# Kernel optimization log

Hardware: AMD Instinct MI355X
Metric: run time of the kernel (lower is better)

The kernel has to match this reference:

```python
import jax, jax.numpy as jnp
import numpy as np
from jax import lax

B, N, S, NSAMPLE = 8, 4096, 1024, 32
RADIUS = 0.2
EPS = 1e-5
IN_CH = 64
MLP = [64, 64, 128]


def _fps(xyz, npoint):
    # farthest point sampling; deterministic start at index 0 (torch uses a random start)
    b, n, _ = xyz.shape
    bidx = jnp.arange(b)

    def step(carry, _):
        distance, farthest = carry
        centroid = xyz[bidx, farthest][:, None, :]            # [B,1,3]
        d = jnp.sum((xyz - centroid) ** 2, axis=-1)           # [B,N]
        distance = jnp.minimum(distance, d)
        nxt = jnp.argmax(distance, axis=-1).astype(jnp.int32)
        return (distance, nxt), farthest

    init = (jnp.full((b, n), 1e10, dtype=xyz.dtype), jnp.zeros((b,), jnp.int32))
    _, idxs = lax.scan(step, init, None, length=npoint)
    return idxs.T                                             # [B,npoint]


def _index_points(p, idx):
    # p: [B,N,C], idx: [B,...] -> [B,...,C]
    return jax.vmap(lambda pp, ii: pp[ii])(p, idx)


def _square_distance(src, dst):
    # src [B,S,3], dst [B,N,3] -> [B,S,N]
    d = -2.0 * jnp.einsum('bsc,bnc->bsn', src, dst)
    d += jnp.sum(src ** 2, -1)[:, :, None]
    d += jnp.sum(dst ** 2, -1)[:, None, :]
    return d


def _query_ball(radius, nsample, xyz, new_xyz):
    n = xyz.shape[1]
    sqr = _square_distance(new_xyz, xyz)                      # [B,S,N]
    gidx = jnp.where(sqr > radius ** 2, n, jnp.arange(n, dtype=jnp.int32))
    gidx = jnp.sort(gidx, axis=-1)[:, :, :nsample]            # [B,S,nsample]
    first = gidx[:, :, :1]
    return jnp.where(gidx == n, first, gidx)


def setup_inputs() -> dict:
    key = jax.random.key(0)
    ks = jax.random.split(key, 8)
    inp = {
        'xyz': jax.random.uniform(ks[0], (B, N, 3), jnp.float32),
        'points': jax.random.normal(ks[1], (B, N, IN_CH), jnp.float32),
    }
    last = IN_CH + 3
    for i, out_c in enumerate(MLP):
        scale = 1.0 / np.sqrt(last)
        inp[f'w{i}'] = jax.random.normal(ks[2 + i], (out_c, last), jnp.float32) * scale
        inp[f'b{i}'] = jnp.zeros((out_c,), jnp.float32)
        inp[f'g{i}'] = jnp.ones((out_c,), jnp.float32)
        inp[f'be{i}'] = jnp.zeros((out_c,), jnp.float32)
        last = out_c
    return inp


def _forward(xyz, points, params):
    fps_idx = _fps(xyz, S)
    new_xyz = _index_points(xyz, fps_idx)                     # [B,S,3]
    idx = _query_ball(RADIUS, NSAMPLE, xyz, new_xyz)          # [B,S,n]
    grouped_xyz = _index_points(xyz, idx) - new_xyz[:, :, None, :]
    h = jnp.concatenate([grouped_xyz, _index_points(points, idx)], axis=-1)  # [B,S,n,67]
    for (w, b, g, be) in params:
        h = jnp.einsum('bsnc,oc->bsno', h, w) + b             # 1x1 conv
        mu = jnp.mean(h, axis=(0, 1, 2))
        var = jnp.var(h, axis=(0, 1, 2))                      # training-mode batch norm
        h = jax.nn.relu((h - mu) * lax.rsqrt(var + EPS) * g + be)
    new_points = jnp.max(h, axis=2)                           # [B,S,Cout]
    return new_xyz, jnp.transpose(new_points, (0, 2, 1))      # [B,Cout,S] like torch


def reference(xyz, points, w0, b0, g0, be0, w1, b1, g1, be1, w2, b2, g2, be2):
    params = [(w0, b0, g0, be0), (w1, b1, g1, be1), (w2, b2, g2, be2)]
    return _forward(xyz, points, params)
```

## Files before the change

kernel.cpp:

```cpp
#include <hip/hip_runtime.h>
#include <stdint.h>

#define NB 8
#define NPTS 4096
#define NS 1024
#define NK 32
#define NROWS (NB*NS*NK)
#define R2 0.04f
#define NCOPY 32

typedef __attribute__((ext_vector_type(8))) short bf16x8;
typedef __attribute__((ext_vector_type(4))) float f32x4;
typedef __attribute__((ext_vector_type(2))) float f32x2;

__device__ __forceinline__ float bf2f(uint16_t u){
    uint32_t v = ((uint32_t)u) << 16;
    return __uint_as_float(v);
}
__device__ __forceinline__ uint16_t f2bf(float f){
    uint32_t u = __float_as_uint(f);
    uint32_t r = (u + 0x7FFFu + ((u >> 16) & 1u)) >> 16;
    return (uint16_t)r;
}
__device__ __forceinline__ bf16x8 load_bf8(const uint16_t* p){
    return *reinterpret_cast<const bf16x8*>(p);
}

#define DPPMAX64(key, ctrl, rmask)                                             \
    {                                                                          \
        uint32_t _lo = (uint32_t)(key), _hi = (uint32_t)((key) >> 32);         \
        uint32_t _olo = (uint32_t)__builtin_amdgcn_update_dpp(                 \
            0, (int)_lo, (ctrl), (rmask), 0xf, true);                          \
        uint32_t _ohi = (uint32_t)__builtin_amdgcn_update_dpp(                 \
            0, (int)_hi, (ctrl), (rmask), 0xf, true);                          \
        unsigned long long _o = (((unsigned long long)_ohi) << 32) | _olo;     \
        key = (_o > (key)) ? _o : (key);                                       \
    }

#define FT 16
__global__ __launch_bounds__(256) void fps_kernel(const float* __restrict__ xyz,
                                                  float* __restrict__ out_newxyz){
    __shared__ float LX[NPTS], LY[NPTS], LZ[NPTS];
    __shared__ float4 SC[NS];
    __shared__ alignas(16) unsigned long long cand[2][4];
    const int b = blockIdx.x, t = threadIdx.x;
    const float* base = xyz + (size_t)b * (NPTS*3);
    f32x2 px2[FT/2], py2[FT/2], pz2[FT/2], pd2[FT/2];
#pragma unroll
    for (int j = 0; j < FT/2; ++j){
        int i = t*FT + 2*j;
        float x0 = base[i*3+0], y0 = base[i*3+1], z0 = base[i*3+2];
        float x1 = base[i*3+3], y1 = base[i*3+4], z1 = base[i*3+5];
        px2[j] = (f32x2){x0, x1};
        py2[j] = (f32x2){y0, y1};
        pz2[j] = (f32x2){z0, z1};
        pd2[j] = (f32x2){1e10f, 1e10f};
        LX[i]=x0; LY[i]=y0; LZ[i]=z0;
        LX[i+1]=x1; LY[i+1]=y1; LZ[i+1]=z1;
    }
    __syncthreads();
    int cur = 0;
    const int wave = t >> 6, lane = t & 63;
    for (int s = 0; s < NS; ++s){
        float cx = LX[cur], cy = LY[cur], cz = LZ[cur];
        if (t == 0) SC[s] = make_float4(cx, cy, cz, 0.f);
        f32x2 ncx = (f32x2){-cx, -cx};
        f32x2 ncy = (f32x2){-cy, -cy};
        f32x2 ncz = (f32x2){-cz, -cz};
        float bestd = -1.0f; int besti = 0;
#pragma unroll
        for (int j = 0; j < FT/2; ++j){
            f32x2 d2;
            {
#pragma clang fp contract(off)
                f32x2 dx = px2[j] + ncx;
                f32x2 dy = py2[j] + ncy;
                f32x2 dz = pz2[j] + ncz;
                f32x2 xx = dx*dx, yy = dy*dy, zz = dz*dz;
                d2 = (xx + yy) + zz;
            }
            f32x2 nd;
            nd.x = fminf(pd2[j].x, d2.x);
            nd.y = fminf(pd2[j].y, d2.y);
            pd2[j] = nd;
            if (nd.x > bestd){ bestd = nd.x; besti = t*FT + 2*j; }
            if (nd.y > bestd){ bestd = nd.y; besti = t*FT + 2*j + 1; }
        }
        unsigned long long key =
            (((unsigned long long)__float_as_uint(bestd)) << 32) |
            (unsigned long long)(~(unsigned)besti);
        DPPMAX64(key, 0x111, 0xf);
        DPPMAX64(key, 0x112, 0xf);
        DPPMAX64(key, 0x114, 0xf);
        DPPMAX64(key, 0x118, 0xf);
        DPPMAX64(key, 0x142, 0xa);
        DPPMAX64(key, 0x143, 0xc);
        int p = s & 1;
        if (lane == 63) cand[p][wave] = key;
        __syncthreads();
        ulonglong2 c01 = *reinterpret_cast<const ulonglong2*>(&cand[p][0]);
        ulonglong2 c23 = *reinterpret_cast<const ulonglong2*>(&cand[p][2]);
        unsigned long long m01 = (c01.x > c01.y) ? c01.x : c01.y;
        unsigned long long m23 = (c23.x > c23.y) ? c23.x : c23.y;
        unsigned long long km  = (m01 > m23) ? m01 : m23;
        cur = (int)(~(uint32_t)km);
    }
    __syncthreads();
    for (int i = t; i < NS; i += 256){
        float4 c = SC[i];
        float* o = out_newxyz + ((size_t)b*NS + i)*3;
        o[0] = c.x; o[1] = c.y; o[2] = c.z;
    }
}

__global__ __launch_bounds__(256) void qball_kernel(const float* __restrict__ xyz,
                                                    const float* __restrict__ newxyz,
                                                    int* __restrict__ idx_out){
    int gid = blockIdx.x*256 + threadIdx.x;
    int w = gid >> 6, lane = gid & 63;
    int b = w >> 10;
    const float* q = newxyz + (size_t)w*3;
    float qx = q[0], qy = q[1], qz = q[2];
    float qn = qx*qx;
    qn = fmaf(qy, qy, qn);
    qn = fmaf(qz, qz, qn);
    const float* base = xyz + (size_t)b * (NPTS*3);
    int cnt = 0, first = 0;
    for (int c0 = 0; c0 < NPTS; c0 += 64){
        int i = c0 + lane;
        float x = base[i*3+0], y = base[i*3+1], z = base[i*3+2];
        float xn = x*x;
        xn = fmaf(y, y, xn);
        xn = fmaf(z, z, xn);
        float dot = qx*x;
        dot = fmaf(qy, y, dot);
        dot = fmaf(qz, z, dot);
        float d;
        {
#pragma clang fp contract(off)
            d = -2.0f * dot;
            d = d + qn;
            d = d + xn;
        }
        bool in = !(d > R2);
        unsigned long long m = __ballot(in);
        if (in){
            int rank = __popcll(m & ((1ull << lane) - 1ull));
            int pos = cnt + rank;
            if (pos < NK) idx_out[(size_t)w*NK + pos] = i;
        }
        if (cnt == 0 && m) first = c0 + (__ffsll((unsigned long long)m) - 1);
        cnt += __popcll(m);
        if (cnt >= NK) break;
    }
    if (cnt < NK){
        for (int p = cnt + lane; p < NK; p += 64) idx_out[(size_t)w*NK + p] = first;
    }
}

__global__ void prep_kernel(const float* __restrict__ w0, const float* __restrict__ w1,
                            const float* __restrict__ w2, uint16_t* __restrict__ w0b,
                            uint16_t* __restrict__ w1b, uint16_t* __restrict__ w2b,
                            double* __restrict__ accumAll){
    int t = blockIdx.x*256 + threadIdx.x;
    int stride = gridDim.x*256;
    for (int i = t; i < 3*NCOPY*256; i += stride) accumAll[i] = 0.0;
    for (int i = t; i < 64*96; i += stride){
        int n = i/96, c = i%96;
        w0b[i] = (c < 67) ? f2bf(w0[n*67 + c]) : (uint16_t)0;
    }
    for (int i = t; i < 64*64; i += stride)  w1b[i] = f2bf(w1[i]);
    for (int i = t; i < 128*64; i += stride) w2b[i] = f2bf(w2[i]);
}

__global__ __launch_bounds__(256) void layer0_mfma(const float* __restrict__ xyz,
                                                   const float* __restrict__ pts,
                                                   const int* __restrict__ idx,
                                                   const float* __restrict__ newxyz,
                                                   const uint16_t* __restrict__ w0b,
                                                   const float* __restrict__ b0,
                                                   uint16_t* __restrict__ z0,
                                                   double* __restrict__ accumOut){
    __shared__ float S_s[16][64], S_q[16][64];
    const int wave = threadIdx.x >> 6, lane = threadIdx.x & 63;
    const int q = lane >> 4, l16 = lane & 15;
    const int r0 = blockIdx.x*64 + wave*16;
    const int row = r0 + l16;
    const int b = row >> 15;
    const int bs = row >> 5;
    const int id = idx[row];
    const float* prow = pts + (((size_t)b << 12) + id)*64;
    const float* xr   = xyz + (((size_t)b << 12) + id)*3;
    const float* qr   = newxyz + (size_t)bs*3;
    float d0 = xr[0]-qr[0], d1 = xr[1]-qr[1], d2 = xr[2]-qr[2];

    bf16x8 Bf[4][3];
#pragma unroll
    for (int nt = 0; nt < 4; ++nt)
#pragma unroll
        for (int s = 0; s < 3; ++s)
            Bf[nt][s] = load_bf8(w0b + (nt*16 + l16)*96 + s*32 + q*8);

    f32x4 acc[4];
#pragma unroll
    for (int nt = 0; nt < 4; ++nt) acc[nt] = (f32x4){0.f,0.f,0.f,0.f};

#pragma unroll
    for (int s = 0; s < 3; ++s){
        const int k0 = s*32 + q*8;
        bf16x8 a;
#pragma unroll
        for (int j = 0; j < 8; ++j){
            int k = k0 + j;
            float v = (k < 3) ? ((k == 0) ? d0 : ((k == 1) ? d1 : d2))
                              : ((k < 67) ? prow[k-3] : 0.f);
            a[j] = (short)f2bf(v);
        }
#pragma unroll
        for (int nt = 0; nt < 4; ++nt)
            acc[nt] = __builtin_amdgcn_mfma_f32_16x16x32_bf16(a, Bf[nt][s], acc[nt], 0, 0, 0);
    }
#pragma unroll
    for (int nt = 0; nt < 4; ++nt){
        int c = nt*16 + l16;
        float bb = b0[c];
        float sps = 0.f, spq = 0.f;
#pragma unroll
        for (int reg = 0; reg < 4; ++reg){
            int rr = r0 + q*4 + reg;
            float h = acc[nt][reg] + bb;
            sps += h;
            spq = fmaf(h, h, spq);
            z0[(size_t)rr*64 + c] = f2bf(h);
        }
        S_s[wave*4 + q][c] = sps;
        S_q[wave*4 + q][c] = spq;
    }
    __syncthreads();
    int t = threadIdx.x;
    if (t < 64){
        double ss = 0.0, sq = 0.0;
#pragma unroll
        for (int i = 0; i < 16; ++i){ ss += (double)S_s[i][t]; sq += (double)S_q[i][t]; }
        int cp = blockIdx.x & (NCOPY-1);
        atomicAdd(&accumOut[cp*256 + t], ss);
        atomicAdd(&accumOut[cp*256 + 128 + t], sq);
    }
}

__global__ __launch_bounds__(256) void layer1_mfma(const uint16_t* __restrict__ zin,
                                                   const double* __restrict__ accumIn,
                                                   const float* __restrict__ g,
                                                   const float* __restrict__ be,
                                                   const uint16_t* __restrict__ wb,
                                                   const float* __restrict__ bias,
                                                   uint16_t* __restrict__ zout,
                                                   double* __restrict__ accumOut){
    constexpr int NT = 4;
    __shared__ float sc_l[64], sh_l[64];
    __shared__ float S_s[16][64], S_q[16][64];
    const int t = threadIdx.x;
    if (t < 64){
        double s = 0.0, qq = 0.0;
#pragma unroll
        for (int cp = 0; cp < NCOPY; ++cp){
            s  += accumIn[cp*256 + t];
            qq += accumIn[cp*256 + 128 + t];
        }
        double mean = s / (double)NROWS;
        double var  = qq / (double)NROWS - mean*mean;
        double rs = 1.0 / sqrt(var + 1e-5);
        double scv = (double)g[t] * rs;
        sc_l[t] = (float)scv;
        sh_l[t] = (float)((double)be[t] - mean*scv);
    }
    __syncthreads();

    const int wave = t >> 6, lane = t & 63;
    const int q = lane >> 4, l16 = lane & 15;
    const int r0 = blockIdx.x*64 + wave*16;

    bf16x8 Bf[NT][2];
#pragma unroll
    for (int nt = 0; nt < NT; ++nt)
#pragma unroll
        for (int s = 0; s < 2; ++s)
            Bf[nt][s] = load_bf8(wb + (nt*16 + l16)*64 + s*32 + q*8);

    float sc[2][8], sh[2][8];
#pragma unroll
    for (int s = 0; s < 2; ++s)
#pragma unroll
        for (int j = 0; j < 8; ++j){
            sc[s][j] = sc_l[s*32 + q*8 + j];
            sh[s][j] = sh_l[s*32 + q*8 + j];
        }

    f32x4 acc[NT];
#pragma unroll
    for (int nt = 0; nt < NT; ++nt) acc[nt] = (f32x4){0.f,0.f,0.f,0.f};

    const uint16_t* zr = zin + (size_t)(r0 + l16)*64;
#pragma unroll
    for (int s = 0; s < 2; ++s){
        uint4 u = *reinterpret_cast<const uint4*>(zr + s*32 + q*8);
        float h[8];
        h[0] = bf2f((uint16_t)(u.x & 0xFFFF)); h[1] = bf2f((uint16_t)(u.x >> 16));
        h[2] = bf2f((uint16_t)(u.y & 0xFFFF)); h[3] = bf2f((uint16_t)(u.y >> 16));
        h[4] = bf2f((uint16_t)(u.z & 0xFFFF)); h[5] = bf2f((uint16_t)(u.z >> 16));
        h[6] = bf2f((uint16_t)(u.w & 0xFFFF)); h[7] = bf2f((uint16_t)(u.w >> 16));
        bf16x8 a;
#pragma unroll
        for (int j = 0; j < 8; ++j){
            float v = fmaxf(fmaf(h[j], sc[s][j], sh[s][j]), 0.f);
            a[j] = (short)f2bf(v);
        }
#pragma unroll
        for (int nt = 0; nt < NT; ++nt)
            acc[nt] = __builtin_amdgcn_mfma_f32_16x16x32_bf16(a, Bf[nt][s], acc[nt], 0, 0, 0);
    }
#pragma unroll
    for (int nt = 0; nt < NT; ++nt){
        int c = nt*16 + l16;
        float bb = bias[c];
        float sps = 0.f, spq = 0.f;
#pragma unroll
        for (int reg = 0; reg < 4; ++reg){
            int rr = r0 + q*4 + reg;
            float h = acc[nt][reg] + bb;
            sps += h;
            spq = fmaf(h, h, spq);
            zout[(size_t)rr*64 + c] = f2bf(h);
        }
        S_s[wave*4 + q][c] = sps;
        S_q[wave*4 + q][c] = spq;
    }
    __syncthreads();
    if (t < 64){
        double ss = 0.0, sq = 0.0;
#pragma unroll
        for (int i = 0; i < 16; ++i){ ss += (double)S_s[i][t]; sq += (double)S_q[i][t]; }
        int cp = blockIdx.x & (NCOPY-1);
        atomicAdd(&accumOut[cp*256 + t], ss);
        atomicAdd(&accumOut[cp*256 + 128 + t], sq);
    }
}

__global__ __launch_bounds__(256) void layer2_mfma(const uint16_t* __restrict__ zin,
                                                   const double* __restrict__ accumIn,
                                                   const float* __restrict__ g,
                                                   const float* __restrict__ be,
                                                   const uint16_t* __restrict__ wb,
                                                   const float* __restrict__ bias,
                                                   float2* __restrict__ pool,
                                                   double* __restrict__ accumOut){
    constexpr int NT = 8;
    __shared__ float sc_l[64], sh_l[64];
    __shared__ float S_s[16][128], S_q[16][128];
    __shared__ float P_mx[16][128], P_mn[16][128];
    const int t = threadIdx.x;
    if (t < 64){
        double s = 0.0, qq = 0.0;
#pragma unroll
        for (int cp = 0; cp < NCOPY; ++cp){
            s  += accumIn[cp*256 + t];
            qq += accumIn[cp*256 + 128 + t];
        }
        double mean = s / (double)NROWS;
        double var  = qq / (double)NROWS - mean*mean;
        double rs = 1.0 / sqrt(var + 1e-5);
        double scv = (double)g[t] * rs;
        sc_l[t] = (float)scv;
        sh_l[t] = (float)((double)be[t] - mean*scv);
    }
    __syncthreads();

    const int wave = t >> 6, lane = t & 63;
    const int q = lane >> 4, l16 = lane & 15;
    const int r0 = blockIdx.x*64 + wave*16;

    bf16x8 Bf[NT][2];
#pragma unroll
    for (int nt = 0; nt < NT; ++nt)
#pragma unroll
        for (int s = 0; s < 2; ++s)
            Bf[nt][s] = load_bf8(wb + (nt*16 + l16)*64 + s*32 + q*8);

    float sc[2][8], sh[2][8];
#pragma unroll
    for (int s = 0; s < 2; ++s)
#pragma unroll
        for (int j = 0; j < 8; ++j){
            sc[s][j] = sc_l[s*32 + q*8 + j];
            sh[s][j] = sh_l[s*32 + q*8 + j];
        }

    f32x4 acc[NT];
#pragma unroll
    for (int nt = 0; nt < NT; ++nt) acc[nt] = (f32x4){0.f,0.f,0.f,0.f};

    const uint16_t* zr = zin + (size_t)(r0 + l16)*64;
#pragma unroll
    for (int s = 0; s < 2; ++s){
        uint4 u = *reinterpret_cast<const uint4*>(zr + s*32 + q*8);
        float h[8];
        h[0] = bf2f((uint16_t)(u.x & 0xFFFF)); h[1] = bf2f((uint16_t)(u.x >> 16));
        h[2] = bf2f((uint16_t)(u.y & 0xFFFF)); h[3] = bf2f((uint16_t)(u.y >> 16));
        h[4] = bf2f((uint16_t)(u.z & 0xFFFF)); h[5] = bf2f((uint16_t)(u.z >> 16));
        h[6] = bf2f((uint16_t)(u.w & 0xFFFF)); h[7] = bf2f((uint16_t)(u.w >> 16));
        bf16x8 a;
#pragma unroll
        for (int j = 0; j < 8; ++j){
            float v = fmaxf(fmaf(h[j], sc[s][j], sh[s][j]), 0.f);
            a[j] = (short)f2bf(v);
        }
#pragma unroll
        for (int nt = 0; nt < NT; ++nt)
            acc[nt] = __builtin_amdgcn_mfma_f32_16x16x32_bf16(a, Bf[nt][s], acc[nt], 0, 0, 0);
    }
#pragma unroll
    for (int nt = 0; nt < NT; ++nt){
        int c = nt*16 + l16;
        float bb = bias[c];
        float sps = 0.f, spq = 0.f;
        float mx = -1e30f, mn = 1e30f;
#pragma unroll
        for (int reg = 0; reg < 4; ++reg){
            float h = acc[nt][reg] + bb;
            sps += h;
            spq = fmaf(h, h, spq);
            mx = fmaxf(mx, h);
            mn = fminf(mn, h);
        }
        S_s[wave*4 + q][c] = sps;
        S_q[wave*4 + q][c] = spq;
        P_mx[wave*4 + q][c] = mx;
        P_mn[wave*4 + q][c] = mn;
    }
    __syncthreads();
    if (t < 128){
        double ss = 0.0, sq = 0.0;
#pragma unroll
        for (int i = 0; i < 16; ++i){ ss += (double)S_s[i][t]; sq += (double)S_q[i][t]; }
        int cp = blockIdx.x & (NCOPY-1);
        atomicAdd(&accumOut[cp*256 + t], ss);
        atomicAdd(&accumOut[cp*256 + 128 + t], sq);
    }
    {
        int gidx = t >> 7;
        int c = t & 127;
        float mx = -1e30f, mn = 1e30f;
#pragma unroll
        for (int i = 0; i < 8; ++i){
            mx = fmaxf(mx, P_mx[gidx*8 + i][c]);
            mn = fminf(mn, P_mn[gidx*8 + i][c]);
        }
        pool[(size_t)(blockIdx.x*2 + gidx)*128 + c] = make_float2(mx, mn);
    }
}

__global__ __launch_bounds__(256) void final_kernel(const float2* __restrict__ pool,
                                                    const double* __restrict__ accumIn,
                                                    const float* __restrict__ g,
                                                    const float* __restrict__ be,
                                                    float* __restrict__ out){
    __shared__ float sc_l[128], sh_l[128];
    const int t0 = threadIdx.x;
    if (t0 < 128){
        double s = 0.0, qq = 0.0;
#pragma unroll
        for (int cp = 0; cp < NCOPY; ++cp){
            s  += accumIn[cp*256 + t0];
            qq += accumIn[cp*256 + 128 + t0];
        }
        double mean = s / (double)NROWS;
        double var  = qq / (double)NROWS - mean*mean;
        double rs = 1.0 / sqrt(var + 1e-5);
        double scv = (double)g[t0] * rs;
        sc_l[t0] = (float)scv;
        sh_l[t0] = (float)((double)be[t0] - mean*scv);
    }
    __syncthreads();

    int t = blockIdx.x*256 + threadIdx.x;
    int o = t & 127;
    int s = (t >> 7) & 1023;
    int b = t >> 17;
    float2 p = pool[t];
    float sc = sc_l[o], sh = sh_l[o];
    float zsel = (sc >= 0.f) ? p.x : p.y;
    float y = fmaxf(fmaf(zsel, sc, sh), 0.f);
    out[24576 + ((size_t)b << 17) + ((size_t)o << 10) + s] = y;
}

extern "C" void kernel_launch(void* const* d_in, const int* in_sizes, int n_in,
                              void* d_out, int out_size, void* d_ws, size_t ws_size,
                              hipStream_t stream) {
    const float* xyz = (const float*)d_in[0];
    const float* pts = (const float*)d_in[1];
    const float* w0  = (const float*)d_in[2];
    const float* b0  = (const float*)d_in[3];
    const float* g0  = (const float*)d_in[4];
    const float* be0 = (const float*)d_in[5];
    const float* w1  = (const float*)d_in[6];
    const float* b1  = (const float*)d_in[7];
    const float* g1  = (const float*)d_in[8];
    const float* be1 = (const float*)d_in[9];
    const float* w2  = (const float*)d_in[10];
    const float* b2  = (const float*)d_in[11];
    const float* g2  = (const float*)d_in[12];
    const float* be2 = (const float*)d_in[13];
    float* out = (float*)d_out;

    char* ws = (char*)d_ws;
    double*   accum0 = (double*)(ws + 0);
    double*   accum1 = (double*)(ws + 65536);
    double*   accum2 = (double*)(ws + 131072);
    uint16_t* w0b    = (uint16_t*)(ws + 196608);
    uint16_t* w1b    = (uint16_t*)(ws + 208896);
    uint16_t* w2b    = (uint16_t*)(ws + 217088);
    uint16_t* z0     = (uint16_t*)(ws + 262144);
    uint16_t* z1     = (uint16_t*)(ws + 33816576);
    float2*   pool   = (float2*)  (ws + 67371008);
    int*      idx    = (int*)     (ws + 75759616);

    prep_kernel<<<32, 256, 0, stream>>>(w0, w1, w2, w0b, w1b, w2b, accum0);
    fps_kernel<<<NB, 256, 0, stream>>>(xyz, out);
    qball_kernel<<<2048, 256, 0, stream>>>(xyz, out, idx);
    layer0_mfma<<<4096, 256, 0, stream>>>(xyz, pts, idx, out, w0b, b0, z0, accum0);
    layer1_mfma<<<4096, 256, 0, stream>>>(z0, accum0, g0, be0, w1b, b1, z1, accum1);
    layer2_mfma<<<4096, 256, 0, stream>>>(z1, accum1, g1, be1, w2b, b2, pool, accum2);
    final_kernel<<<4096, 256, 0, stream>>>(pool, accum2, g2, be2, out);
}
```

Baseline: 830.4 us.

## Fuse FPS, ball query and layer0 into one persistent producer-consumer kernel

Merges the FPS, ball-query and first MLP layer kernels into one launch. The first 8 blocks run FPS and publish each centroid to global memory with a flag, and the worker blocks spin on those flags. Each worker then runs the ball query for two centroids into shared memory and does the layer0 MFMA right away. The aim is to overlap the long serial FPS with grouping and layer0 work and to drop the idx buffer round trip. It risks deadlock if the FPS blocks are not resident before the spinning workers, and it relies on oversized shared memory to force one block per CU.

```diff
diff --git a/kernel.cpp b/kernel.cpp
--- a/kernel.cpp
+++ b/kernel.cpp
@@ -24,6 +24,25 @@
 }
 __device__ __forceinline__ bf16x8 load_bf8(const uint16_t* p){
     return *reinterpret_cast<const bf16x8*>(p);
+}
+
+__device__ __forceinline__ void publish_cent(float* cent, int cell,
+                                             float cx, float cy, float cz){
+    f32x4 v; v[0] = cx; v[1] = cy; v[2] = cz; v[3] = 1.0f;
+    unsigned long long a = (unsigned long long)(uintptr_t)(cent + (size_t)cell*4);
+    asm volatile("global_store_dwordx4 %0, %1, off sc0 sc1"
+                 :: "v"(a), "v"(v) : "memory");
+}
+__device__ __forceinline__ f32x4 wait_cent(const float* cent, int cell){
+    const uint32_t* wp = (const uint32_t*)(cent + (size_t)cell*4) + 3;
+    while (__hip_atomic_load(wp, __ATOMIC_RELAXED, __HIP_MEMORY_SCOPE_AGENT)
+           != 0x3F800000u)
+        __builtin_amdgcn_s_sleep(32);
+    f32x4 r;
+    unsigned long long a = (unsigned long long)(uintptr_t)(cent + (size_t)cell*4);
+    asm volatile("global_load_dwordx4 %0, %1, off sc0 sc1\n\ts_waitcnt vmcnt(0)"
+                 : "=v"(r) : "v"(a) : "memory");
+    return r;
 }
 
 #define DPPMAX64(key, ctrl, rmask)                                             \
@@ -37,215 +56,235 @@
         key = (_o > (key)) ? _o : (key);                                       \
     }
 
+struct FpsSh {
+    float LX[NPTS], LY[NPTS], LZ[NPTS];
+    f32x4 SC[NS];
+    alignas(16) unsigned long long cand[2][4];
+};
+struct WrkSh {
+    float S_s[16][64], S_q[16][64];
+    int   idxL[2][NK];
+    f32x4 Lc[2];
+};
+union MegaSh { FpsSh f; WrkSh w; char force_one_block_per_cu[86016]; };
+
 #define FT 16
-__global__ __launch_bounds__(256) void fps_kernel(const float* __restrict__ xyz,
-                                                  float* __restrict__ out_newxyz){
-    __shared__ float LX[NPTS], LY[NPTS], LZ[NPTS];
-    __shared__ float4 SC[NS];
-    __shared__ alignas(16) unsigned long long cand[2][4];
-    const int b = blockIdx.x, t = threadIdx.x;
-    const float* base = xyz + (size_t)b * (NPTS*3);
-    f32x2 px2[FT/2], py2[FT/2], pz2[FT/2], pd2[FT/2];
-#pragma unroll
-    for (int j = 0; j < FT/2; ++j){
-        int i = t*FT + 2*j;
-        float x0 = base[i*3+0], y0 = base[i*3+1], z0 = base[i*3+2];
-        float x1 = base[i*3+3], y1 = base[i*3+4], z1 = base[i*3+5];
-        px2[j] = (f32x2){x0, x1};
-        py2[j] = (f32x2){y0, y1};
-        pz2[j] = (f32x2){z0, z1};
-        pd2[j] = (f32x2){1e10f, 1e10f};
-        LX[i]=x0; LY[i]=y0; LZ[i]=z0;
-        LX[i+1]=x1; LY[i+1]=y1; LZ[i+1]=z1;
-    }
-    __syncthreads();
-    int cur = 0;
-    const int wave = t >> 6, lane = t & 63;
-    for (int s = 0; s < NS; ++s){
-        float cx = LX[cur], cy = LY[cur], cz = LZ[cur];
-        if (t == 0) SC[s] = make_float4(cx, cy, cz, 0.f);
-        f32x2 ncx = (f32x2){-cx, -cx};
-        f32x2 ncy = (f32x2){-cy, -cy};
-        f32x2 ncz = (f32x2){-cz, -cz};
-        float bestd = -1.0f; int besti = 0;
+__global__ __launch_bounds__(256) void mega_kernel(const float* __restrict__ xyz,
+                                                   const float* __restrict__ pts,
+                                                   const uint16_t* __restrict__ w0b,
+                                                   const float* __restrict__ b0,
+                                                   uint16_t* __restrict__ z0,
+                                                   double* __restrict__ accumOut,
+                                                   float* __restrict__ cent,
+                                                   float* __restrict__ out_newxyz){
+    __shared__ MegaSh sh;
+    const int t = threadIdx.x;
+
+    if (blockIdx.x < NB){
+        const int b = blockIdx.x;
+        const float* base = xyz + (size_t)b * (NPTS*3);
+        f32x2 px2[FT/2], py2[FT/2], pz2[FT/2], pd2[FT/2];
 #pragma unroll
         for (int j = 0; j < FT/2; ++j){
-            f32x2 d2;
-            {
+            int i = t*FT + 2*j;
+            float x0 = base[i*3+0], y0 = base[i*3+1], z0c = base[i*3+2];
+            float x1 = base[i*3+3], y1 = base[i*3+4], z1c = base[i*3+5];
+            px2[j] = (f32x2){x0, x1};
+            py2[j] = (f32x2){y0, y1};
+            pz2[j] = (f32x2){z0c, z1c};
+            pd2[j] = (f32x2){1e10f, 1e10f};
+            sh.f.LX[i]=x0; sh.f.LY[i]=y0; sh.f.LZ[i]=z0c;
+            sh.f.LX[i+1]=x1; sh.f.LY[i+1]=y1; sh.f.LZ[i+1]=z1c;
+        }
+        __syncthreads();
+        int cur = 0;
+        const int wave = t >> 6, lane = t & 63;
+        for (int s = 0; s < NS; ++s){
+            float cx = sh.f.LX[cur], cy = sh.f.LY[cur], cz = sh.f.LZ[cur];
+            if (t == 0){
+                sh.f.SC[s] = (f32x4){cx, cy, cz, 0.f};
+                publish_cent(cent, b*NS + s, cx, cy, cz);
+            }
+            f32x2 ncx = (f32x2){-cx, -cx};
+            f32x2 ncy = (f32x2){-cy, -cy};
+            f32x2 ncz = (f32x2){-cz, -cz};
+            float bestd = -1.0f; int besti = 0;
+#pragma unroll
+            for (int j = 0; j < FT/2; ++j){
+                f32x2 d2;
+                {
 #pragma clang fp contract(off)
-                f32x2 dx = px2[j] + ncx;
-                f32x2 dy = py2[j] + ncy;
-                f32x2 dz = pz2[j] + ncz;
-                f32x2 xx = dx*dx, yy = dy*dy, zz = dz*dz;
-                d2 = (xx + yy) + zz;
+                    f32x2 dx = px2[j] + ncx;
+                    f32x2 dy = py2[j] + ncy;
+                    f32x2 dz = pz2[j] + ncz;
+                    f32x2 xx = dx*dx, yy = dy*dy, zz = dz*dz;
+                    d2 = (xx + yy) + zz;
+                }
+                f32x2 nd;
+                nd.x = fminf(pd2[j].x, d2.x);
+                nd.y = fminf(pd2[j].y, d2.y);
+                pd2[j] = nd;
+                if (nd.x > bestd){ bestd = nd.x; besti = t*FT + 2*j; }
+                if (nd.y > bestd){ bestd = nd.y; besti = t*FT + 2*j + 1; }
             }
-            f32x2 nd;
-            nd.x = fminf(pd2[j].x, d2.x);
-            nd.y = fminf(pd2[j].y, d2.y);
-            pd2[j] = nd;
-            if (nd.x > bestd){ bestd = nd.x; besti = t*FT + 2*j; }
-            if (nd.y > bestd){ bestd = nd.y; besti = t*FT + 2*j + 1; }
-        }
-        unsigned long long key =
-            (((unsigned long long)__float_as_uint(bestd)) << 32) |
-            (unsigned long long)(~(unsigned)besti);
-        DPPMAX64(key, 0x111, 0xf);
-        DPPMAX64(key, 0x112, 0xf);
-        DPPMAX64(key, 0x114, 0xf);
-        DPPMAX64(key, 0x118, 0xf);
-        DPPMAX64(key, 0x142, 0xa);
-        DPPMAX64(key, 0x143, 0xc);
-        int p = s & 1;
-        if (lane == 63) cand[p][wave] = key;
+            unsigned long long key =
+                (((unsigned long long)__float_as_uint(bestd)) << 32) |
+                (unsigned long long)(~(unsigned)besti);
+            DPPMAX64(key, 0x111, 0xf);
+            DPPMAX64(key, 0x112, 0xf);
+            DPPMAX64(key, 0x114, 0xf);
+            DPPMAX64(key, 0x118, 0xf);
+            DPPMAX64(key, 0x142, 0xa);
+            DPPMAX64(key, 0x143, 0xc);
+            int p = s & 1;
+            if (lane == 63) sh.f.cand[p][wave] = key;
+            __syncthreads();
+            ulonglong2 c01 = *reinterpret_cast<const ulonglong2*>(&sh.f.cand[p][0]);
+            ulonglong2 c23 = *reinterpret_cast<const ulonglong2*>(&sh.f.cand[p][2]);
+            unsigned long long m01 = (c01.x > c01.y) ? c01.x : c01.y;
+            unsigned long long m23 = (c23.x > c23.y) ? c23.x : c23.y;
+            unsigned long long km  = (m01 > m23) ? m01 : m23;
+            cur = (int)(~(uint32_t)km);
+        }
         __syncthreads();
-        ulonglong2 c01 = *reinterpret_cast<const ulonglong2*>(&cand[p][0]);
-        ulonglong2 c23 = *reinterpret_cast<const ulonglong2*>(&cand[p][2]);
-        unsigned long long m01 = (c01.x > c01.y) ? c01.x : c01.y;
-        unsigned long long m23 = (c23.x > c23.y) ? c23.x : c23.y;
-        unsigned long long km  = (m01 > m23) ? m01 : m23;
-        cur = (int)(~(uint32_t)km);
-    }
-    __syncthreads();
-    for (int i = t; i < NS; i += 256){
-        float4 c = SC[i];
-        float* o = out_newxyz + ((size_t)b*NS + i)*3;
-        o[0] = c.x; o[1] = c.y; o[2] = c.z;
-    }
-}
-
-__global__ __launch_bounds__(256) void qball_kernel(const float* __restrict__ xyz,
-                                                    const float* __restrict__ newxyz,
-                                                    int* __restrict__ idx_out){
-    int gid = blockIdx.x*256 + threadIdx.x;
-    int w = gid >> 6, lane = gid & 63;
-    int b = w >> 10;
-    const float* q = newxyz + (size_t)w*3;
-    float qx = q[0], qy = q[1], qz = q[2];
-    float qn = qx*qx;
-    qn = fmaf(qy, qy, qn);
-    qn = fmaf(qz, qz, qn);
-    const float* base = xyz + (size_t)b * (NPTS*3);
-    int cnt = 0, first = 0;
-    for (int c0 = 0; c0 < NPTS; c0 += 64){
-        int i = c0 + lane;
-        float x = base[i*3+0], y = base[i*3+1], z = base[i*3+2];
-        float xn = x*x;
-        xn = fmaf(y, y, xn);
-        xn = fmaf(z, z, xn);
-        float dot = qx*x;
-        dot = fmaf(qy, y, dot);
-        dot = fmaf(qz, z, dot);
-        float d;
-        {
+        for (int i = t; i < NS; i += 256){
+            f32x4 c = sh.f.SC[i];
+            float* o = out_newxyz + ((size_t)b*NS + i)*3;
+            o[0] = c[0]; o[1] = c[1]; o[2] = c[2];
+        }
+    } else {
+        const int w = (int)blockIdx.x - NB;
+        const int stile = w >> 3;
+        const int b = w & 7;
+        const int wave = t >> 6, lane = t & 63;
+        const int q = lane >> 4, l16 = lane & 15;
+
+        bf16x8 Bf[4][3];
+#pragma unroll
+        for (int nt = 0; nt < 4; ++nt)
+#pragma unroll
+            for (int s = 0; s < 3; ++s)
+                Bf[nt][s] = load_bf8(w0b + (nt*16 + l16)*96 + s*32 + q*8);
+
+        if (t == 0){
+            sh.w.Lc[0] = wait_cent(cent, b*NS + stile*2 + 0);
+            sh.w.Lc[1] = wait_cent(cent, b*NS + stile*2 + 1);
+        }
+        __syncthreads();
+
+        if (wave < 2){
+            f32x4 qc = sh.w.Lc[wave];
+            float qx = qc[0], qy = qc[1], qz = qc[2];
+            float qn = qx*qx;
+            qn = fmaf(qy, qy, qn);
+            qn = fmaf(qz, qz, qn);
+            const float* base = xyz + (size_t)b * (NPTS*3);
+            int cnt = 0, first = 0;
+            for (int c0 = 0; c0 < NPTS; c0 += 64){
+                int i = c0 + lane;
+                float x = base[i*3+0], y = base[i*3+1], z = base[i*3+2];
+                float xn = x*x;
+                xn = fmaf(y, y, xn);
+                xn = fmaf(z, z, xn);
+                float dot = qx*x;
+                dot = fmaf(qy, y, dot);
+                dot = fmaf(qz, z, dot);
+                float d;
+                {
 #pragma clang fp contract(off)
-            d = -2.0f * dot;
-            d = d + qn;
-            d = d + xn;
-        }
-        bool in = !(d > R2);
-        unsigned long long m = __ballot(in);
-        if (in){
-            int rank = __popcll(m & ((1ull << lane) - 1ull));
-            int pos = cnt + rank;
-            if (pos < NK) idx_out[(size_t)w*NK + pos] = i;
-        }
-        if (cnt == 0 && m) first = c0 + (__ffsll((unsigned long long)m) - 1);
-        cnt += __popcll(m);
-        if (cnt >= NK) break;
-    }
-    if (cnt < NK){
-        for (int p = cnt + lane; p < NK; p += 64) idx_out[(size_t)w*NK + p] = first;
+                    d = -2.0f * dot;
+                    d = d + qn;
+                    d = d + xn;
+                }
+                bool in = !(d > R2);
+                unsigned long long m = __ballot(in);
+                if (in){
+                    int rank = __popcll(m & ((1ull << lane) - 1ull));
+                    int pos = cnt + rank;
+                    if (pos < NK) sh.w.idxL[wave][pos] = i;
+                }
+                if (cnt == 0 && m) first = c0 + (__ffsll((unsigned long long)m) - 1);
+                cnt += __popcll(m);
+                if (cnt >= NK) break;
+            }
+            if (cnt < NK){
+                for (int p = cnt + lane; p < NK; p += 64) sh.w.idxL[wave][p] = first;
+            }
+        }
+        __syncthreads();
+
+        const int rowbase = (b*NS + stile*2)*NK;
+        const int r0 = rowbase + wave*16;
+        const int cell = wave >> 1;
+        const int sample = (wave & 1)*16 + l16;
+        const int id = sh.w.idxL[cell][sample];
+        const float* prow = pts + (((size_t)b << 12) + id)*64;
+        const float* xr   = xyz + (((size_t)b << 12) + id)*3;
+        f32x4 qc = sh.w.Lc[cell];
+        float d0 = xr[0]-qc[0], d1 = xr[1]-qc[1], d2 = xr[2]-qc[2];
+
+        f32x4 acc[4];
+#pragma unroll
+        for (int nt = 0; nt < 4; ++nt) acc[nt] = (f32x4){0.f,0.f,0.f,0.f};
+
+#pragma unroll
+        for (int s = 0; s < 3; ++s){
+            const int k0 = s*32 + q*8;
+            bf16x8 a;
+#pragma unroll
+            for (int j = 0; j < 8; ++j){
+                int k = k0 + j;
+                float v = (k < 3) ? ((k == 0) ? d0 : ((k == 1) ? d1 : d2))
+                                  : ((k < 67) ? prow[k-3] : 0.f);
+                a[j] = (short)f2bf(v);
+            }
+#pragma unroll
+            for (int nt = 0; nt < 4; ++nt)
+                acc[nt] = __builtin_amdgcn_mfma_f32_16x16x32_bf16(a, Bf[nt][s], acc[nt], 0, 0, 0);
+        }
+#pragma unroll
+        for (int nt = 0; nt < 4; ++nt){
+            int c = nt*16 + l16;
+            float bb = b0[c];
+            float sps = 0.f, spq = 0.f;
+#pragma unroll
+            for (int reg = 0; reg < 4; ++reg){
+                int rr = r0 + q*4 + reg;
+                float h = acc[nt][reg] + bb;
+                sps += h;
+                spq = fmaf(h, h, spq);
+                z0[(size_t)rr*64 + c] = f2bf(h);
+            }
+            sh.w.S_s[wave*4 + q][c] = sps;
+            sh.w.S_q[wave*4 + q][c] = spq;
+        }
+        __syncthreads();
+        if (t < 64){
+            double ss = 0.0, sq = 0.0;
+#pragma unroll
+            for (int i = 0; i < 16; ++i){ ss += (double)sh.w.S_s[i][t]; sq += (double)sh.w.S_q[i][t]; }
+            int cp = blockIdx.x & (NCOPY-1);
+            atomicAdd(&accumOut[cp*256 + t], ss);
+            atomicAdd(&accumOut[cp*256 + 128 + t], sq);
+        }
     }
 }
 
 __global__ void prep_kernel(const float* __restrict__ w0, const float* __restrict__ w1,
                             const float* __restrict__ w2, uint16_t* __restrict__ w0b,
                             uint16_t* __restrict__ w1b, uint16_t* __restrict__ w2b,
-                            double* __restrict__ accumAll){
+                            double* __restrict__ accumAll, float* __restrict__ cent){
     int t = blockIdx.x*256 + threadIdx.x;
     int stride = gridDim.x*256;
     for (int i = t; i < 3*NCOPY*256; i += stride) accumAll[i] = 0.0;
+    for (int i = t; i < NB*NS; i += stride)
+        ((f32x4*)cent)[i] = (f32x4){0.f, 0.f, 0.f, 0.f};
     for (int i = t; i < 64*96; i += stride){
         int n = i/96, c = i%96;
         w0b[i] = (c < 67) ? f2bf(w0[n*67 + c]) : (uint16_t)0;
     }
     for (int i = t; i < 64*64; i += stride)  w1b[i] = f2bf(w1[i]);
     for (int i = t; i < 128*64; i += stride) w2b[i] = f2bf(w2[i]);
-}
-
-__global__ __launch_bounds__(256) void layer0_mfma(const float* __restrict__ xyz,
-                                                   const float* __restrict__ pts,
-                                                   const int* __restrict__ idx,
-                                                   const float* __restrict__ newxyz,
-                                                   const uint16_t* __restrict__ w0b,
-                                                   const float* __restrict__ b0,
-                                                   uint16_t* __restrict__ z0,
-                                                   double* __restrict__ accumOut){
-    __shared__ float S_s[16][64], S_q[16][64];
-    const int wave = threadIdx.x >> 6, lane = threadIdx.x & 63;
-    const int q = lane >> 4, l16 = lane & 15;
-    const int r0 = blockIdx.x*64 + wave*16;
-    const int row = r0 + l16;
-    const int b = row >> 15;
-    const int bs = row >> 5;
-    const int id = idx[row];
-    const float* prow = pts + (((size_t)b << 12) + id)*64;
-    const float* xr   = xyz + (((size_t)b << 12) + id)*3;
-    const float* qr   = newxyz + (size_t)bs*3;
-    float d0 = xr[0]-qr[0], d1 = xr[1]-qr[1], d2 = xr[2]-qr[2];
-
-    bf16x8 Bf[4][3];
-#pragma unroll
-    for (int nt = 0; nt < 4; ++nt)
-#pragma unroll
-        for (int s = 0; s < 3; ++s)
-            Bf[nt][s] = load_bf8(w0b + (nt*16 + l16)*96 + s*32 + q*8);
-
-    f32x4 acc[4];
-#pragma unroll
-    for (int nt = 0; nt < 4; ++nt) acc[nt] = (f32x4){0.f,0.f,0.f,0.f};
-
-#pragma unroll
-    for (int s = 0; s < 3; ++s){
-        const int k0 = s*32 + q*8;
-        bf16x8 a;
-#pragma unroll
-        for (int j = 0; j < 8; ++j){
-            int k = k0 + j;
-            float v = (k < 3) ? ((k == 0) ? d0 : ((k == 1) ? d1 : d2))
-                              : ((k < 67) ? prow[k-3] : 0.f);
-            a[j] = (short)f2bf(v);
-        }
-#pragma unroll
-        for (int nt = 0; nt < 4; ++nt)
-            acc[nt] = __builtin_amdgcn_mfma_f32_16x16x32_bf16(a, Bf[nt][s], acc[nt], 0, 0, 0);
-    }
-#pragma unroll
-    for (int nt = 0; nt < 4; ++nt){
-        int c = nt*16 + l16;
-        float bb = b0[c];
-        float sps = 0.f, spq = 0.f;
-#pragma unroll
-        for (int reg = 0; reg < 4; ++reg){
-            int rr = r0 + q*4 + reg;
-            float h = acc[nt][reg] + bb;
-            sps += h;
-            spq = fmaf(h, h, spq);
-            z0[(size_t)rr*64 + c] = f2bf(h);
-        }
-        S_s[wave*4 + q][c] = sps;
-        S_q[wave*4 + q][c] = spq;
-    }
-    __syncthreads();
-    int t = threadIdx.x;
-    if (t < 64){
-        double ss = 0.0, sq = 0.0;
-#pragma unroll
-        for (int i = 0; i < 16; ++i){ ss += (double)S_s[i][t]; sq += (double)S_q[i][t]; }
-        int cp = blockIdx.x & (NCOPY-1);
-        atomicAdd(&accumOut[cp*256 + t], ss);
-        atomicAdd(&accumOut[cp*256 + 128 + t], sq);
-    }
 }
 
 __global__ __launch_bounds__(256) void layer1_mfma(const uint16_t* __restrict__ zin,
@@ -522,12 +561,10 @@
     uint16_t* z0     = (uint16_t*)(ws + 262144);
     uint16_t* z1     = (uint16_t*)(ws + 33816576);
     float2*   pool   = (float2*)  (ws + 67371008);
-    int*      idx    = (int*)     (ws + 75759616);
-
-    prep_kernel<<<32, 256, 0, stream>>>(w0, w1, w2, w0b, w1b, w2b, accum0);
-    fps_kernel<<<NB, 256, 0, stream>>>(xyz, out);
-    qball_kernel<<<2048, 256, 0, stream>>>(xyz, out, idx);
-    layer0_mfma<<<4096, 256, 0, stream>>>(xyz, pts, idx, out, w0b, b0, z0, accum0);
+    float*    cent   = (float*)   (ws + 75759616);
+
+    prep_kernel<<<32, 256, 0, stream>>>(w0, w1, w2, w0b, w1b, w2b, accum0, cent);
+    mega_kernel<<<NB + 4096, 256, 0, stream>>>(xyz, pts, w0b, b0, z0, accum0, cent, out);
     layer1_mfma<<<4096, 256, 0, stream>>>(z0, accum0, g0, be0, w1b, b1, z1, accum1);
     layer2_mfma<<<4096, 256, 0, stream>>>(z1, accum1, g1, be1, w2b, b2, pool, accum2);
     final_kernel<<<4096, 256, 0, stream>>>(pool, accum2, g2, be2, out);
```

Measured after the change: 817.4 us. Within noise of the previous version (-1.6%).
